# Performance work log

Hardware: AMD Instinct MI355X
Metric: run time of the kernel (lower is better)

## Reference

```python
import jax, jax.numpy as jnp
import numpy as np

B, C, D, Hh, W = 2, 320, 4, 16, 16
N = D * Hh * W          # 1024 nodes
NH = 8                  # num_heads
DH = C // NH            # 40
L = 2                   # num_layers
A, EPD = 16, 64         # da_prior tokens, encode_prior_dim
EDGE_SCALE = 32 ** -0.5 # GraphEdgeFeature dim_head=32
SCALE = DH ** -0.5
EPS = 1e-5


def _ln(x, g, b):
    m = x.mean(-1, keepdims=True)
    v = ((x - m) ** 2).mean(-1, keepdims=True)
    return (x - m) * jax.lax.rsqrt(v + EPS) * g + b


def setup_inputs() -> dict:
    key = jax.random.key(0)
    ks = jax.random.split(key, 16)
    std = 0.02 / np.sqrt(L)
    inp = {
        'x': jax.random.normal(ks[0], (B, C, D, Hh, W), jnp.float32),
        'da_prior': jax.random.normal(ks[1], (B, A, EPD), jnp.float32),
        # GraphEdgeFeature.to_qk (no bias), init std 0.02/sqrt(24)
        'qk_w': jax.random.normal(ks[2], (2 * C, C), jnp.float32) * (0.02 / np.sqrt(24)),
        # fc_prior
        'fcp_w': jax.random.normal(ks[3], (C, EPD), jnp.float32) * 0.02,
        'fcp_b': jnp.zeros((C,), jnp.float32),
        # per-layer (stacked over L)
        'ln1_g': jnp.ones((L, C), jnp.float32),
        'ln1_b': jnp.zeros((L, C), jnp.float32),
        'gln_g': jnp.ones((L, C), jnp.float32),
        'gln_b': jnp.zeros((L, C), jnp.float32),
        'qkv_w': jax.random.normal(ks[4], (L, 3 * C, C), jnp.float32) * std,
        'qkv_b': jnp.zeros((L, 3 * C), jnp.float32),
        'proj_w': jax.random.normal(ks[5], (L, C, C), jnp.float32) * std,
        'proj_b': jnp.zeros((L, C), jnp.float32),
        # expand Conv2d(1, NH, 1): weight [NH], bias [NH]
        'exp_w': jax.random.normal(ks[6], (L, NH), jnp.float32),
        'exp_b': jnp.zeros((L, NH), jnp.float32),
        # reduce Conv2d(NH, 1, 1): weight [NH], bias scalar
        'red_w': jax.random.normal(ks[7], (L, NH), jnp.float32) / np.sqrt(NH),
        'red_b': jnp.zeros((L,), jnp.float32),
    }
    return inp


def _forward(x, da_prior, qk_w, fcp_w, fcp_b, ln1_g, ln1_b, gln_g, gln_b,
             qkv_w, qkv_b, proj_w, proj_b, exp_w, exp_b, red_w, red_b):
    node = x.reshape(B, C, N)                       # [B,C,N]
    # ---- GraphEdgeFeature: full-dim QK attention over nodes ----
    xt = node.transpose(0, 2, 1)                    # [B,N,C]
    qk = xt @ qk_w.T                                # [B,N,2C]
    q_e, k_e = jnp.split(qk, 2, axis=-1)
    edge = jax.nn.softmax(jnp.einsum('bqc,bkc->bqk', q_e, k_e) * EDGE_SCALE, axis=-1)  # [B,N,N]
    # ---- fc_prior ----
    da = da_prior @ fcp_w.T + fcp_b                 # [B,A,C]
    s = da.sum(axis=1)                              # [B,C] (sum over 'a' in einsum bnc,bca->bnc)
    for l in range(L):
        # block norm1 over channel dim
        nt = _ln(node.transpose(0, 2, 1), ln1_g[l], ln1_b[l])   # [B,N,C]
        # torch.einsum('bnn,bnc->bnc') takes the DIAGONAL of edge
        diag = jnp.diagonal(edge, axis1=1, axis2=2)             # [B,N]
        node2 = diag[:, :, None] * nt * s[:, None, :] + nt      # [B,N,C]
        y = _ln(node2, gln_g[l], gln_b[l])
        qkv = (y @ qkv_w[l].T + qkv_b[l]).reshape(B, N, 3, NH, DH)
        qkv = qkv.transpose(2, 0, 3, 1, 4)                      # [3,B,H,N,DH]
        q, k, v = qkv[0], qkv[1], qkv[2]
        attn = jnp.einsum('bhnd,bhmd->bhnm', q, k) * SCALE
        attn = attn + edge[:, None] * exp_w[l][None, :, None, None] + exp_b[l][None, :, None, None]
        a = jax.nn.softmax(attn, axis=-1)                       # [B,H,N,N]
        node_out = jnp.einsum('bhnm,bhmd->bhnd', a, v).transpose(0, 2, 1, 3).reshape(B, N, C)
        edge_new = jnp.einsum('bhnm,h->bnm', a + attn, red_w[l]) + red_b[l]  # [B,N,N]
        ws = jax.nn.softmax(edge_new, axis=-1)
        wsum = (ws * edge_new).sum(-1)                          # [B,N]
        node_out = node_out + wsum[:, :, None]                  # fc=Identity, broadcast
        node_out = node_out @ proj_w[l].T + proj_b[l]
        node = node_out.transpose(0, 2, 1)                      # [B,C,N]
        edge = edge + edge_new
    return node.reshape(B, C, D, Hh, W)


def reference(x, da_prior, qk_w, fcp_w, fcp_b, ln1_g, ln1_b, gln_g, gln_b,
              qkv_w, qkv_b, proj_w, proj_b, exp_w, exp_b, red_w, red_b):
    return _forward(x, da_prior, qk_w, fcp_w, fcp_b, ln1_g, ln1_b, gln_g, gln_b,
                    qkv_w, qkv_b, proj_w, proj_b, exp_w, exp_b, red_w, red_b)
```

## Files before the change

### kernel.cpp

```cpp
#include <hip/hip_runtime.h>
#include <math.h>

#define EDGE_SCALE 0.17677669529663687f
#define ATT_SCALE  0.15811388300841897f
#define LN_EPS 1e-5f

typedef __attribute__((ext_vector_type(8))) short bf8;
typedef __attribute__((ext_vector_type(4))) float f32x4;

__device__ __forceinline__ f32x4 mfma16(bf8 a, bf8 b, f32x4 c) {
  return __builtin_amdgcn_mfma_f32_16x16x32_bf16(a, b, c, 0, 0, 0);
}
__device__ __forceinline__ unsigned short f2bf(float f) {
  union { float f; unsigned u; } v; v.f = f;
  unsigned r = v.u + 0x7FFF + ((v.u >> 16) & 1);
  return (unsigned short)(r >> 16);
}
__device__ __forceinline__ float bf2f(unsigned short h) {
  union { unsigned u; float f; } v; v.u = ((unsigned)h) << 16;
  return v.f;
}
__device__ __forceinline__ float wave_max(float v) {
  #pragma unroll
  for (int o = 32; o > 0; o >>= 1) v = fmaxf(v, __shfl_xor(v, o));
  return v;
}
__device__ __forceinline__ float wave_sum(float v) {
  #pragma unroll
  for (int o = 32; o > 0; o >>= 1) v += __shfl_xor(v, o);
  return v;
}

__global__ __launch_bounds__(256) void k_trans(const float* __restrict__ x,
    float* __restrict__ node, unsigned short* __restrict__ nodebf) {
  __shared__ float tile[32][33];
  const int b = blockIdx.z;
  const int n0 = blockIdx.x * 32, c0 = blockIdx.y * 32;
  const int tx = threadIdx.x & 31, ty = threadIdx.x >> 5;
  #pragma unroll
  for (int k = 0; k < 4; ++k) {
    int c = c0 + ty + 8 * k;
    tile[ty + 8 * k][tx] = x[((size_t)b * 320 + c) * 1024 + n0 + tx];
  }
  __syncthreads();
  #pragma unroll
  for (int k = 0; k < 4; ++k) {
    int n = n0 + ty + 8 * k;
    float v = tile[tx][ty + 8 * k];
    size_t idx = ((size_t)b * 1024 + n) * 320 + c0 + tx;
    node[idx] = v;
    nodebf[idx] = f2bf(v);
  }
}

__global__ __launch_bounds__(320) void k_svec(const float* __restrict__ da,
    const float* __restrict__ fw, const float* __restrict__ fb, float* __restrict__ sv) {
  __shared__ float ds[64];
  const int b = blockIdx.x, t = threadIdx.x;
  if (t < 64) {
    float a = 0.f;
    #pragma unroll
    for (int i = 0; i < 16; ++i) a += da[b * 1024 + i * 64 + t];
    ds[t] = a;
  }
  __syncthreads();
  if (t < 320) {
    float acc = 16.f * fb[t];
    #pragma unroll
    for (int e = 0; e < 64; ++e) acc = fmaf(ds[e], fw[t * 64 + e], acc);
    sv[b * 320 + t] = acc;
  }
}

__global__ void k_wcvt(const float* __restrict__ a, int na,
                       const float* __restrict__ b, int nb,
                       const float* __restrict__ c, int nc,
                       unsigned short* __restrict__ out) {
  int tot = na + nb + nc;
  for (int i = blockIdx.x * blockDim.x + threadIdx.x; i < tot; i += gridDim.x * blockDim.x) {
    float v = (i < na) ? a[i] : ((i < na + nb) ? b[i - na] : c[i - na - nb]);
    out[i] = f2bf(v);
  }
}

__global__ __launch_bounds__(256, 4) void k_mgemm(
    const unsigned short* __restrict__ A, const unsigned short* __restrict__ W,
    const float* __restrict__ bias, void* p0, void* p1, void* p2, int mode) {
  __shared__ float smem[64 * 65];
  const int t = threadIdx.x, w = t >> 6, lane = t & 63;
  const int q16 = lane >> 4, l16 = lane & 15;
  const int rt = blockIdx.x * 64, jt = blockIdx.y * 64;
  f32x4 acc[4];
  #pragma unroll
  for (int i = 0; i < 4; ++i)
    #pragma unroll
    for (int j = 0; j < 4; ++j) acc[i][j] = 0.f;
  const unsigned short* ap = A + (size_t)(rt + 16 * w + l16) * 320 + q16 * 8;
  const unsigned short* wp = W + (size_t)(jt + l16) * 320 + q16 * 8;
  for (int kc = 0; kc < 10; ++kc) {
    bf8 af = *(const bf8*)(ap + kc * 32);
    #pragma unroll
    for (int ct = 0; ct < 4; ++ct) {
      bf8 bf = *(const bf8*)(wp + (size_t)ct * 16 * 320 + kc * 32);
      acc[ct] = mfma16(af, bf, acc[ct]);
    }
  }
  if (mode == 0 || mode == 1) {
    #pragma unroll
    for (int ct = 0; ct < 4; ++ct) {
      int col = jt + ct * 16 + l16;
      float bv = bias ? bias[col] : 0.f;
      #pragma unroll
      for (int r = 0; r < 4; ++r) {
        int row = rt + 16 * w + q16 * 4 + r;
        float v = acc[ct][r] + bv;
        if (mode == 0) {
          ((float*)p0)[(size_t)row * 320 + col] = v;
        } else {
          if (col < 320) ((unsigned short*)p0)[(size_t)row * 320 + col] = f2bf(v);
          else           ((unsigned short*)p1)[(size_t)row * 320 + col - 320] = f2bf(v);
        }
      }
    }
  } else if (mode == 2) {
    const int part = jt / 320;
    if (part < 2) {
      unsigned short* dst = (unsigned short*)(part == 0 ? p0 : p1);
      #pragma unroll
      for (int ct = 0; ct < 4; ++ct) {
        int col = jt + ct * 16 + l16;
        float bv = bias[col];
        int rem = col - part * 320;
        int h = rem / 40, d = rem % 40;
        #pragma unroll
        for (int r = 0; r < 4; ++r) {
          int row = rt + 16 * w + q16 * 4 + r;
          int b = row >> 10, n = row & 1023;
          size_t base = (((size_t)b * 8 + h) * 1024 + n) * 64;
          dst[base + d] = f2bf(acc[ct][r] + bv);
          if (d < 24) dst[base + 40 + d] = 0;
        }
      }
    } else {
      unsigned short* vt_t = (unsigned short*)smem;
      #pragma unroll
      for (int ct = 0; ct < 4; ++ct) {
        int col = jt + ct * 16 + l16;
        float bv = bias[col];
        #pragma unroll
        for (int r = 0; r < 4; ++r)
          vt_t[(ct * 16 + l16) * 72 + 16 * w + q16 * 4 + r] = f2bf(acc[ct][r] + bv);
      }
      __syncthreads();
      const int cl = t >> 2, seg = t & 3;
      int rem = (jt - 640) + cl;
      int h = rem / 40, d = rem % 40;
      int b = rt >> 10, n = (rt & 1023) + seg * 16;
      const float4* lp = (const float4*)&vt_t[cl * 72 + seg * 16];
      float4 a0 = lp[0], a1 = lp[1];
      float4* gp = (float4*)((unsigned short*)p2 +
                             (((size_t)b * 8 + h) * 48 + d) * 1024 + n);
      gp[0] = a0; gp[1] = a1;
    }
  } else {
    #pragma unroll
    for (int ct = 0; ct < 4; ++ct) {
      int col = jt + ct * 16 + l16;
      float bv = bias[col];
      #pragma unroll
      for (int r = 0; r < 4; ++r)
        smem[(16 * w + q16 * 4 + r) * 65 + ct * 16 + l16] = acc[ct][r] + bv;
    }
    __syncthreads();
    const int cl = t >> 2, seg = t & 3;
    int b = rt >> 10, n = (rt & 1023) + seg * 16;
    float* orow = (float*)p0 + ((size_t)b * 320 + jt + cl) * 1024 + n;
    #pragma unroll
    for (int i2 = 0; i2 < 4; ++i2) {
      float4 vv;
      vv.x = smem[(seg * 16 + i2 * 4 + 0) * 65 + cl];
      vv.y = smem[(seg * 16 + i2 * 4 + 1) * 65 + cl];
      vv.z = smem[(seg * 16 + i2 * 4 + 2) * 65 + cl];
      vv.w = smem[(seg * 16 + i2 * 4 + 3) * 65 + cl];
      ((float4*)orow)[i2] = vv;
    }
  }
}

__global__ __launch_bounds__(256, 4) void k_sgemm(
    const unsigned short* __restrict__ qe, const unsigned short* __restrict__ ke,
    float* __restrict__ S) {
  const int t = threadIdx.x, w = t >> 6, lane = t & 63;
  const int q16 = lane >> 4, l16 = lane & 15;
  const int rt = blockIdx.x * 64, jt = blockIdx.y * 64, b = blockIdx.z;
  const unsigned short* A = qe + (size_t)b * 1024 * 320;
  const unsigned short* W = ke + (size_t)b * 1024 * 320;
  f32x4 acc[4];
  #pragma unroll
  for (int i = 0; i < 4; ++i)
    #pragma unroll
    for (int j = 0; j < 4; ++j) acc[i][j] = 0.f;
  const unsigned short* ap = A + (size_t)(rt + 16 * w + l16) * 320 + q16 * 8;
  const unsigned short* wp = W + (size_t)(jt + l16) * 320 + q16 * 8;
  for (int kc = 0; kc < 10; ++kc) {
    bf8 af = *(const bf8*)(ap + kc * 32);
    #pragma unroll
    for (int ct = 0; ct < 4; ++ct) {
      bf8 bf = *(const bf8*)(wp + (size_t)ct * 16 * 320 + kc * 32);
      acc[ct] = mfma16(af, bf, acc[ct]);
    }
  }
  #pragma unroll
  for (int ct = 0; ct < 4; ++ct)
    #pragma unroll
    for (int r = 0; r < 4; ++r)
      S[((size_t)b * 1024 + rt + 16 * w + q16 * 4 + r) * 1024 + jt + ct * 16 + l16] =
          acc[ct][r] * EDGE_SCALE;
}

__global__ __launch_bounds__(256) void k_smax(const float* __restrict__ S,
                                              float* __restrict__ edge) {
  const int w = threadIdx.x >> 6, lane = threadIdx.x & 63;
  const int row = blockIdx.x * 4 + w;
  const float4* sp = (const float4*)(S + (size_t)row * 1024) + lane;
  float4 v[4];
  #pragma unroll
  for (int i = 0; i < 4; ++i) v[i] = sp[i * 64];
  float mx = -3.4e38f;
  #pragma unroll
  for (int i = 0; i < 4; ++i)
    mx = fmaxf(mx, fmaxf(fmaxf(v[i].x, v[i].y), fmaxf(v[i].z, v[i].w)));
  mx = wave_max(mx);
  float s = 0.f;
  #pragma unroll
  for (int i = 0; i < 4; ++i) {
    v[i].x = __expf(v[i].x - mx); v[i].y = __expf(v[i].y - mx);
    v[i].z = __expf(v[i].z - mx); v[i].w = __expf(v[i].w - mx);
    s += v[i].x + v[i].y + v[i].z + v[i].w;
  }
  s = wave_sum(s);
  float inv = 1.f / s;
  float4* ep = (float4*)(edge + (size_t)row * 1024) + lane;
  #pragma unroll
  for (int i = 0; i < 4; ++i)
    ep[i * 64] = make_float4(v[i].x * inv, v[i].y * inv, v[i].z * inv, v[i].w * inv);
}

__global__ __launch_bounds__(256) void k_ln(const float* __restrict__ node,
    const float* __restrict__ edge, const float* __restrict__ sv,
    const float* __restrict__ g1, const float* __restrict__ b1,
    const float* __restrict__ g2, const float* __restrict__ b2,
    unsigned short* __restrict__ y) {
  const int w = threadIdx.x >> 6, lane = threadIdx.x & 63;
  const int row = blockIdx.x * 4 + w;
  const int b = row >> 10, n = row & 1023;
  const float* xr = node + (size_t)row * 320;
  float x[5];
  #pragma unroll
  for (int i = 0; i < 5; ++i) x[i] = xr[lane + 64 * i];
  float s = x[0] + x[1] + x[2] + x[3] + x[4];
  float mean = wave_sum(s) * (1.f / 320.f);
  float v = 0.f;
  #pragma unroll
  for (int i = 0; i < 5; ++i) { float d = x[i] - mean; v += d * d; }
  float rstd = rsqrtf(wave_sum(v) * (1.f / 320.f) + LN_EPS);
  float diag = edge[(size_t)row * 1024 + n];
  float n2[5];
  #pragma unroll
  for (int i = 0; i < 5; ++i) {
    int c = lane + 64 * i;
    float nt = (x[i] - mean) * rstd * g1[c] + b1[c];
    n2[i] = diag * nt * sv[b * 320 + c] + nt;
  }
  s = n2[0] + n2[1] + n2[2] + n2[3] + n2[4];
  float mean2 = wave_sum(s) * (1.f / 320.f);
  v = 0.f;
  #pragma unroll
  for (int i = 0; i < 5; ++i) { float d = n2[i] - mean2; v += d * d; }
  float rstd2 = rsqrtf(wave_sum(v) * (1.f / 320.f) + LN_EPS);
  unsigned short* yr = y + (size_t)row * 320;
  #pragma unroll
  for (int i = 0; i < 5; ++i) {
    int c = lane + 64 * i;
    yr[c] = f2bf((n2[i] - mean2) * rstd2 * g2[c] + b2[c]);
  }
}

__global__ __launch_bounds__(256, 4) void k_score(
    const unsigned short* __restrict__ qbf, const unsigned short* __restrict__ kbf,
    const unsigned short* __restrict__ vtb, const float* __restrict__ edge,
    unsigned short* __restrict__ thbuf, float* __restrict__ att,
    const float* __restrict__ ew, const float* __restrict__ eb,
    const float* __restrict__ rw) {
  __shared__ unsigned short a_lds[4][4][16][20];
  __shared__ unsigned short th_lds[4][16][72];
  __shared__ float ored[4][3][16][17];
  __shared__ float redm[4][16], reds[4][16];
  const int t = threadIdx.x, w = t >> 6, lane = t & 63;
  const int q16 = lane >> 4, l16 = lane & 15;
  const int n0 = blockIdx.x * 16, h = blockIdx.y, b = blockIdx.z;
  const size_t bh = (size_t)b * 8 + h;
  const unsigned short* qp = qbf + (bh * 1024 + n0 + l16) * 64 + q16 * 8;
  bf8 af0 = *(const bf8*)(qp);
  bf8 af1 = *(const bf8*)(qp + 32);
  f32x4 acc[16];
  #pragma unroll
  for (int i = 0; i < 16; ++i)
    #pragma unroll
    for (int j = 0; j < 4; ++j) acc[i][j] = 0.f;
  const unsigned short* kp = kbf + (bh * 1024 + (size_t)w * 256 + l16) * 64 + q16 * 8;
  #pragma unroll
  for (int tt = 0; tt < 16; ++tt) {
    const unsigned short* kpt = kp + (size_t)tt * 16 * 64;
    bf8 b0 = *(const bf8*)(kpt);
    bf8 b1 = *(const bf8*)(kpt + 32);
    acc[tt] = mfma16(af0, b0, acc[tt]);
    acc[tt] = mfma16(af1, b1, acc[tt]);
  }
  const float ewh = ew[h], ebh = eb[h], rwh = rw[h];
  const float* ep = edge + ((size_t)b * 1024 + n0 + q16 * 4) * 1024 + w * 256 + l16;
  #pragma unroll
  for (int tt = 0; tt < 16; ++tt)
    #pragma unroll
    for (int r = 0; r < 4; ++r) {
      float ev = ep[(size_t)r * 1024 + tt * 16];
      acc[tt][r] = fmaf(acc[tt][r], ATT_SCALE, fmaf(ev, ewh, ebh));
    }
  float pm[4] = {-3.4e38f, -3.4e38f, -3.4e38f, -3.4e38f};
  #pragma unroll
  for (int tt = 0; tt < 16; ++tt)
    #pragma unroll
    for (int r = 0; r < 4; ++r) pm[r] = fmaxf(pm[r], acc[tt][r]);
  #pragma unroll
  for (int r = 0; r < 4; ++r)
    #pragma unroll
    for (int o = 1; o <= 8; o <<= 1) pm[r] = fmaxf(pm[r], __shfl_xor(pm[r], o));
  if (l16 == 0) {
    #pragma unroll
    for (int r = 0; r < 4; ++r) redm[w][q16 * 4 + r] = pm[r];
  }
  __syncthreads();
  float m[4], ps[4] = {0.f, 0.f, 0.f, 0.f};
  #pragma unroll
  for (int r = 0; r < 4; ++r)
    m[r] = fmaxf(fmaxf(redm[0][q16 * 4 + r], redm[1][q16 * 4 + r]),
                 fmaxf(redm[2][q16 * 4 + r], redm[3][q16 * 4 + r]));
  #pragma unroll
  for (int tt = 0; tt < 16; ++tt)
    #pragma unroll
    for (int r = 0; r < 4; ++r) ps[r] += __expf(acc[tt][r] - m[r]);
  #pragma unroll
  for (int r = 0; r < 4; ++r)
    #pragma unroll
    for (int o = 1; o <= 8; o <<= 1) ps[r] += __shfl_xor(ps[r], o);
  if (l16 == 0) {
    #pragma unroll
    for (int r = 0; r < 4; ++r) reds[w][q16 * 4 + r] = ps[r];
  }
  __syncthreads();
  float inv[4];
  #pragma unroll
  for (int r = 0; r < 4; ++r)
    inv[r] = 1.f / (reds[0][q16 * 4 + r] + reds[1][q16 * 4 + r] +
                    reds[2][q16 * 4 + r] + reds[3][q16 * 4 + r]);
  f32x4 oacc[3];
  #pragma unroll
  for (int i = 0; i < 3; ++i)
    #pragma unroll
    for (int j = 0; j < 4; ++j) oacc[i][j] = 0.f;
  unsigned short* tbase = thbuf + (bh * 1024 + n0) * 1024 + w * 256;
  const int trow = lane >> 2, tc4 = lane & 3;
  #pragma unroll
  for (int g = 0; g < 4; ++g) {
    #pragma unroll
    for (int ti = 0; ti < 4; ++ti) {
      int tt = g * 4 + ti;
      #pragma unroll
      for (int r = 0; r < 4; ++r) {
        float e = __expf(acc[tt][r] - m[r]);
        float a = e * inv[r];
        a_lds[w][ti][q16 * 4 + r][l16] = f2bf(a);
        th_lds[w][q16 * 4 + r][ti * 16 + l16] = f2bf(rwh * (a + acc[tt][r]));
      }
    }
    #pragma unroll
    for (int kk = 0; kk < 2; ++kk) {
      const unsigned short* ap2 = &a_lds[w][kk * 2 + (q16 >> 1)][l16][(q16 & 1) * 8];
      short4 lo = *(const short4*)(ap2);
      short4 hi = *(const short4*)(ap2 + 4);
      bf8 afv = {lo.x, lo.y, lo.z, lo.w, hi.x, hi.y, hi.z, hi.w};
      int kc = w * 8 + g * 2 + kk;
      const unsigned short* vp = vtb + (bh * 48 + l16) * 1024 + (size_t)kc * 32 + q16 * 8;
      #pragma unroll
      for (int nt = 0; nt < 3; ++nt) {
        bf8 bfv = *(const bf8*)(vp + (size_t)nt * 16 * 1024);
        oacc[nt] = mfma16(afv, bfv, oacc[nt]);
      }
    }
    {
      const float4* lp = (const float4*)&th_lds[w][trow][tc4 * 16];
      float4 v0 = lp[0], v1 = lp[1];
      float4* gp = (float4*)(tbase + (size_t)trow * 1024 + g * 64 + tc4 * 16);
      gp[0] = v0; gp[1] = v1;
    }
  }
  #pragma unroll
  for (int nt = 0; nt < 3; ++nt)
    #pragma unroll
    for (int r = 0; r < 4; ++r) ored[w][nt][q16 * 4 + r][l16] = oacc[nt][r];
  __syncthreads();
  #pragma unroll
  for (int k = 0; k < 3; ++k) {
    int o = k * 256 + t;
    int nt = o >> 8, row = (o >> 4) & 15, col = o & 15;
    int dim = nt * 16 + col;
    float sum = ored[0][nt][row][col] + ored[1][nt][row][col] +
                ored[2][nt][row][col] + ored[3][nt][row][col];
    if (dim < 40)
      att[((size_t)b * 1024 + n0 + row) * 320 + h * 40 + dim] = sum;
  }
}

__global__ __launch_bounds__(256) void k_wsum(
    const unsigned short* __restrict__ thbuf, float* __restrict__ edge,
    const float* __restrict__ att, unsigned short* __restrict__ attbf,
    const float* __restrict__ rb) {
  const int w = threadIdx.x >> 6, lane = threadIdx.x & 63;
  const int row = blockIdx.x * 4 + w;
  const int b = row >> 10, n = row & 1023;
  const float rbv = rb[0];
  float tv[16];
  #pragma unroll
  for (int i = 0; i < 16; ++i) tv[i] = rbv;
  #pragma unroll 1
  for (int h = 0; h < 8; ++h) {
    const unsigned short* tph = thbuf + (((size_t)b * 8 + h) * 1024 + n) * 1024 + lane * 4;
    #pragma unroll
    for (int seg = 0; seg < 4; ++seg) {
      ushort4 u = *(const ushort4*)(tph + seg * 256);
      tv[seg * 4 + 0] += bf2f(u.x);
      tv[seg * 4 + 1] += bf2f(u.y);
      tv[seg * 4 + 2] += bf2f(u.z);
      tv[seg * 4 + 3] += bf2f(u.w);
    }
  }
  float4* erp = (float4*)(edge + ((size_t)b * 1024 + n) * 1024) + lane;
  #pragma unroll
  for (int seg = 0; seg < 4; ++seg) {
    float4 e = erp[seg * 64];
    e.x += tv[seg * 4 + 0]; e.y += tv[seg * 4 + 1];
    e.z += tv[seg * 4 + 2]; e.w += tv[seg * 4 + 3];
    erp[seg * 64] = e;
  }
  float mx = -3.4e38f;
  #pragma unroll
  for (int i = 0; i < 16; ++i) mx = fmaxf(mx, tv[i]);
  mx = wave_max(mx);
  float s = 0.f, num = 0.f;
  #pragma unroll
  for (int i = 0; i < 16; ++i) {
    float e = __expf(tv[i] - mx);
    s += e; num += e * tv[i];
  }
  s = wave_sum(s); num = wave_sum(num);
  const float wsum = num / s;
  const float* ar = att + (size_t)row * 320;
  unsigned short* ao = attbf + (size_t)row * 320;
  #pragma unroll
  for (int i = 0; i < 5; ++i) {
    int c = lane + 64 * i;
    ao[c] = f2bf(ar[c] + wsum);
  }
}

extern "C" void kernel_launch(void* const* d_in, const int* in_sizes, int n_in,
                              void* d_out, int out_size, void* d_ws, size_t ws_size,
                              hipStream_t stream) {
  const float* x      = (const float*)d_in[0];
  const float* da     = (const float*)d_in[1];
  const float* qk_w   = (const float*)d_in[2];
  const float* fcp_w  = (const float*)d_in[3];
  const float* fcp_b  = (const float*)d_in[4];
  const float* ln1_g  = (const float*)d_in[5];
  const float* ln1_b  = (const float*)d_in[6];
  const float* gln_g  = (const float*)d_in[7];
  const float* gln_b  = (const float*)d_in[8];
  const float* qkv_w  = (const float*)d_in[9];
  const float* qkv_b  = (const float*)d_in[10];
  const float* proj_w = (const float*)d_in[11];
  const float* proj_b = (const float*)d_in[12];
  const float* exp_w  = (const float*)d_in[13];
  const float* exp_b  = (const float*)d_in[14];
  const float* red_w  = (const float*)d_in[15];
  const float* red_b  = (const float*)d_in[16];
  float* ws = (float*)d_ws;
  float* node  = ws + 0;
  unsigned short* ybf   = (unsigned short*)(ws + 655360);
  float* attb  = ws + 983040;
  unsigned short* attbf = (unsigned short*)(ws + 1638400);
  float* edge  = ws + 1966080;
  float* svec  = ws + 4063232;
  unsigned short* nodebf = (unsigned short*)(ws + 4063872);
  unsigned short* qe   = (unsigned short*)(ws + 4391552);
  unsigned short* ke   = (unsigned short*)(ws + 4719232);
  unsigned short* qbf  = (unsigned short*)(ws + 5046912);
  unsigned short* kbf  = (unsigned short*)(ws + 5571200);
  unsigned short* vtb  = (unsigned short*)(ws + 6095488);
  unsigned short* wbf  = (unsigned short*)(ws + 6488704);
  unsigned short* thbuf= (unsigned short*)(ws + 7000704);
  float* sbuf = ws + 15389312;
  float* out = (float*)d_out;
  unsigned short* qk_wb   = wbf;
  unsigned short* qkv_wb  = wbf + 204800;
  unsigned short* proj_wb = wbf + 819200;

  hipLaunchKernelGGL(k_trans, dim3(32, 10, 2), dim3(256), 0, stream, x, node, nodebf);
  hipLaunchKernelGGL(k_svec, dim3(2), dim3(320), 0, stream, da, fcp_w, fcp_b, svec);
  hipLaunchKernelGGL(k_wcvt, dim3(512), dim3(256), 0, stream,
                     qk_w, 204800, qkv_w, 614400, proj_w, 204800, wbf);
  hipLaunchKernelGGL(k_mgemm, dim3(32, 10), dim3(256), 0, stream,
                     nodebf, qk_wb, (const float*)nullptr, qe, ke, (void*)nullptr, 1);
  hipLaunchKernelGGL(k_sgemm, dim3(16, 16, 2), dim3(256), 0, stream, qe, ke, sbuf);
  hipLaunchKernelGGL(k_smax, dim3(512), dim3(256), 0, stream, sbuf, edge);
  for (int l = 0; l < 2; ++l) {
    hipLaunchKernelGGL(k_ln, dim3(512), dim3(256), 0, stream, node, edge, svec,
                       ln1_g + l * 320, ln1_b + l * 320, gln_g + l * 320, gln_b + l * 320, ybf);
    hipLaunchKernelGGL(k_mgemm, dim3(32, 15), dim3(256), 0, stream,
                       ybf, qkv_wb + (size_t)l * 307200, qkv_b + l * 960, qbf, kbf, vtb, 2);
    hipLaunchKernelGGL(k_score, dim3(64, 8, 2), dim3(256), 0, stream,
                       qbf, kbf, vtb, edge, thbuf, attb,
                       exp_w + l * 8, exp_b + l * 8, red_w + l * 8);
    hipLaunchKernelGGL(k_wsum, dim3(512), dim3(256), 0, stream,
                       thbuf, edge, attb, attbf, red_b + l);
    if (l == 0)
      hipLaunchKernelGGL(k_mgemm, dim3(32, 5), dim3(256), 0, stream,
                         attbf, proj_wb, proj_b, node, (void*)nullptr, (void*)nullptr, 0);
    else
      hipLaunchKernelGGL(k_mgemm, dim3(32, 5), dim3(256), 0, stream,
                         attbf, proj_wb + 102400, proj_b + 320, out,
                         (void*)nullptr, (void*)nullptr, 3);
  }
}
```

Measured before the change: 293.5 us.

## Fuse edge score GEMM with softmax, pair heads in score kernel, drop max pass

The initial edge QK GEMM and its row softmax are fused into one kernel, so the fp32 score matrix is never written to or read back from memory. The score kernel now handles two heads per block and sums their reduce-weighted contributions in registers, which halves the per-head intermediate traffic into the weighted-sum kernel. Both softmaxes skip the max-subtraction pass, removing one reduction and barrier, at the risk of exp overflow if scores are large. Zeroing of the q/k head padding moves from every GEMM epilogue into a one-time clear inside the weight-conversion kernel.

```diff
diff --git a/kernel.cpp b/kernel.cpp
--- a/kernel.cpp
+++ b/kernel.cpp
@@ -75,12 +75,16 @@
 __global__ void k_wcvt(const float* __restrict__ a, int na,
                        const float* __restrict__ b, int nb,
                        const float* __restrict__ c, int nc,
-                       unsigned short* __restrict__ out) {
+                       unsigned short* __restrict__ out,
+                       uint4* __restrict__ zbuf, int zn4) {
   int tot = na + nb + nc;
   for (int i = blockIdx.x * blockDim.x + threadIdx.x; i < tot; i += gridDim.x * blockDim.x) {
     float v = (i < na) ? a[i] : ((i < na + nb) ? b[i - na] : c[i - na - nb]);
     out[i] = f2bf(v);
   }
+  const uint4 z = {0u, 0u, 0u, 0u};
+  for (int i = blockIdx.x * blockDim.x + threadIdx.x; i < zn4; i += gridDim.x * blockDim.x)
+    zbuf[i] = z;
 }
 
 __global__ __launch_bounds__(256, 4) void k_mgemm(
@@ -136,9 +140,7 @@
         for (int r = 0; r < 4; ++r) {
           int row = rt + 16 * w + q16 * 4 + r;
           int b = row >> 10, n = row & 1023;
-          size_t base = (((size_t)b * 8 + h) * 1024 + n) * 64;
-          dst[base + d] = f2bf(acc[ct][r] + bv);
-          if (d < 24) dst[base + 40 + d] = 0;
+          dst[(((size_t)b * 8 + h) * 1024 + n) * 64 + d] = f2bf(acc[ct][r] + bv);
         }
       }
     } else {
@@ -187,63 +189,64 @@
   }
 }
 
-__global__ __launch_bounds__(256, 4) void k_sgemm(
+__global__ __launch_bounds__(512, 2) void k_edge3(
     const unsigned short* __restrict__ qe, const unsigned short* __restrict__ ke,
-    float* __restrict__ S) {
+    float* __restrict__ edge) {
+  __shared__ float zred[8][16];
   const int t = threadIdx.x, w = t >> 6, lane = t & 63;
   const int q16 = lane >> 4, l16 = lane & 15;
-  const int rt = blockIdx.x * 64, jt = blockIdx.y * 64, b = blockIdx.z;
-  const unsigned short* A = qe + (size_t)b * 1024 * 320;
-  const unsigned short* W = ke + (size_t)b * 1024 * 320;
-  f32x4 acc[4];
-  #pragma unroll
-  for (int i = 0; i < 4; ++i)
+  const int n0 = blockIdx.x * 16, b = blockIdx.y;
+  const unsigned short* qp = qe + ((size_t)(b * 1024 + n0 + l16)) * 320 + q16 * 8;
+  bf8 af[10];
+  #pragma unroll
+  for (int kc = 0; kc < 10; ++kc) af[kc] = *(const bf8*)(qp + kc * 32);
+  f32x4 acc[8];
+  #pragma unroll
+  for (int i = 0; i < 8; ++i)
     #pragma unroll
     for (int j = 0; j < 4; ++j) acc[i][j] = 0.f;
-  const unsigned short* ap = A + (size_t)(rt + 16 * w + l16) * 320 + q16 * 8;
-  const unsigned short* wp = W + (size_t)(jt + l16) * 320 + q16 * 8;
-  for (int kc = 0; kc < 10; ++kc) {
-    bf8 af = *(const bf8*)(ap + kc * 32);
-    #pragma unroll
-    for (int ct = 0; ct < 4; ++ct) {
-      bf8 bf = *(const bf8*)(wp + (size_t)ct * 16 * 320 + kc * 32);
-      acc[ct] = mfma16(af, bf, acc[ct]);
-    }
-  }
-  #pragma unroll
-  for (int ct = 0; ct < 4; ++ct)
-    #pragma unroll
-    for (int r = 0; r < 4; ++r)
-      S[((size_t)b * 1024 + rt + 16 * w + q16 * 4 + r) * 1024 + jt + ct * 16 + l16] =
-          acc[ct][r] * EDGE_SCALE;
-}
-
-__global__ __launch_bounds__(256) void k_smax(const float* __restrict__ S,
-                                              float* __restrict__ edge) {
-  const int w = threadIdx.x >> 6, lane = threadIdx.x & 63;
-  const int row = blockIdx.x * 4 + w;
-  const float4* sp = (const float4*)(S + (size_t)row * 1024) + lane;
-  float4 v[4];
-  #pragma unroll
-  for (int i = 0; i < 4; ++i) v[i] = sp[i * 64];
-  float mx = -3.4e38f;
-  #pragma unroll
-  for (int i = 0; i < 4; ++i)
-    mx = fmaxf(mx, fmaxf(fmaxf(v[i].x, v[i].y), fmaxf(v[i].z, v[i].w)));
-  mx = wave_max(mx);
-  float s = 0.f;
-  #pragma unroll
-  for (int i = 0; i < 4; ++i) {
-    v[i].x = __expf(v[i].x - mx); v[i].y = __expf(v[i].y - mx);
-    v[i].z = __expf(v[i].z - mx); v[i].w = __expf(v[i].w - mx);
-    s += v[i].x + v[i].y + v[i].z + v[i].w;
-  }
-  s = wave_sum(s);
-  float inv = 1.f / s;
-  float4* ep = (float4*)(edge + (size_t)row * 1024) + lane;
-  #pragma unroll
-  for (int i = 0; i < 4; ++i)
-    ep[i * 64] = make_float4(v[i].x * inv, v[i].y * inv, v[i].z * inv, v[i].w * inv);
+  const unsigned short* kp = ke + ((size_t)(b * 1024 + w * 128 + l16)) * 320 + q16 * 8;
+  #pragma unroll
+  for (int mt = 0; mt < 8; ++mt) {
+    const unsigned short* kpt = kp + (size_t)mt * 16 * 320;
+    #pragma unroll
+    for (int kc = 0; kc < 10; ++kc) {
+      bf8 bf = *(const bf8*)(kpt + kc * 32);
+      acc[mt] = mfma16(af[kc], bf, acc[mt]);
+    }
+  }
+  float zp[4] = {0.f, 0.f, 0.f, 0.f};
+  #pragma unroll
+  for (int mt = 0; mt < 8; ++mt)
+    #pragma unroll
+    for (int r = 0; r < 4; ++r) {
+      float e = __expf(acc[mt][r] * EDGE_SCALE);
+      acc[mt][r] = e;
+      zp[r] += e;
+    }
+  #pragma unroll
+  for (int r = 0; r < 4; ++r)
+    #pragma unroll
+    for (int o = 1; o <= 8; o <<= 1) zp[r] += __shfl_xor(zp[r], o);
+  if (l16 == 0) {
+    #pragma unroll
+    for (int r = 0; r < 4; ++r) zred[w][q16 * 4 + r] = zp[r];
+  }
+  __syncthreads();
+  float inv[4];
+  #pragma unroll
+  for (int r = 0; r < 4; ++r) {
+    float s = 0.f;
+    #pragma unroll
+    for (int ww = 0; ww < 8; ++ww) s += zred[ww][q16 * 4 + r];
+    inv[r] = 1.f / s;
+  }
+  #pragma unroll
+  for (int r = 0; r < 4; ++r) {
+    float* ep = edge + ((size_t)(b * 1024 + n0 + q16 * 4 + r)) * 1024 + w * 128 + l16;
+    #pragma unroll
+    for (int mt = 0; mt < 8; ++mt) ep[mt * 16] = acc[mt][r] * inv[r];
+  }
 }
 
 __global__ __launch_bounds__(256) void k_ln(const float* __restrict__ node,
@@ -286,143 +289,139 @@
   }
 }
 
-__global__ __launch_bounds__(256, 4) void k_score(
+__global__ __launch_bounds__(256, 2) void k_score2(
     const unsigned short* __restrict__ qbf, const unsigned short* __restrict__ kbf,
     const unsigned short* __restrict__ vtb, const float* __restrict__ edge,
-    unsigned short* __restrict__ thbuf, float* __restrict__ att,
+    unsigned short* __restrict__ th, float* __restrict__ att,
     const float* __restrict__ ew, const float* __restrict__ eb,
     const float* __restrict__ rw) {
   __shared__ unsigned short a_lds[4][4][16][20];
-  __shared__ unsigned short th_lds[4][16][72];
-  __shared__ float ored[4][3][16][17];
-  __shared__ float redm[4][16], reds[4][16];
+  __shared__ float ored[2][4][3][16][17];
+  __shared__ float zred[2][4][16];
   const int t = threadIdx.x, w = t >> 6, lane = t & 63;
   const int q16 = lane >> 4, l16 = lane & 15;
-  const int n0 = blockIdx.x * 16, h = blockIdx.y, b = blockIdx.z;
-  const size_t bh = (size_t)b * 8 + h;
-  const unsigned short* qp = qbf + (bh * 1024 + n0 + l16) * 64 + q16 * 8;
-  bf8 af0 = *(const bf8*)(qp);
-  bf8 af1 = *(const bf8*)(qp + 32);
-  f32x4 acc[16];
-  #pragma unroll
-  for (int i = 0; i < 16; ++i)
-    #pragma unroll
-    for (int j = 0; j < 4; ++j) acc[i][j] = 0.f;
-  const unsigned short* kp = kbf + (bh * 1024 + (size_t)w * 256 + l16) * 64 + q16 * 8;
-  #pragma unroll
-  for (int tt = 0; tt < 16; ++tt) {
-    const unsigned short* kpt = kp + (size_t)tt * 16 * 64;
-    bf8 b0 = *(const bf8*)(kpt);
-    bf8 b1 = *(const bf8*)(kpt + 32);
-    acc[tt] = mfma16(af0, b0, acc[tt]);
-    acc[tt] = mfma16(af1, b1, acc[tt]);
-  }
-  const float ewh = ew[h], ebh = eb[h], rwh = rw[h];
-  const float* ep = edge + ((size_t)b * 1024 + n0 + q16 * 4) * 1024 + w * 256 + l16;
+  const int n0 = blockIdx.x * 16, hp = blockIdx.y, b = blockIdx.z;
+  float t_reg[16][4];
   #pragma unroll
   for (int tt = 0; tt < 16; ++tt)
     #pragma unroll
-    for (int r = 0; r < 4; ++r) {
-      float ev = ep[(size_t)r * 1024 + tt * 16];
-      acc[tt][r] = fmaf(acc[tt][r], ATT_SCALE, fmaf(ev, ewh, ebh));
-    }
-  float pm[4] = {-3.4e38f, -3.4e38f, -3.4e38f, -3.4e38f};
-  #pragma unroll
-  for (int tt = 0; tt < 16; ++tt)
-    #pragma unroll
-    for (int r = 0; r < 4; ++r) pm[r] = fmaxf(pm[r], acc[tt][r]);
-  #pragma unroll
-  for (int r = 0; r < 4; ++r)
-    #pragma unroll
-    for (int o = 1; o <= 8; o <<= 1) pm[r] = fmaxf(pm[r], __shfl_xor(pm[r], o));
-  if (l16 == 0) {
-    #pragma unroll
-    for (int r = 0; r < 4; ++r) redm[w][q16 * 4 + r] = pm[r];
-  }
+    for (int r = 0; r < 4; ++r) t_reg[tt][r] = 0.f;
+  f32x4 oacc[2][3];
+  #pragma unroll
+  for (int hh = 0; hh < 2; ++hh)
+    #pragma unroll
+    for (int i = 0; i < 3; ++i)
+      #pragma unroll
+      for (int j = 0; j < 4; ++j) oacc[hh][i][j] = 0.f;
+  const float* ep = edge + ((size_t)(b * 1024 + n0 + q16 * 4)) * 1024 + w * 256 + l16;
+  #pragma unroll 1
+  for (int hh = 0; hh < 2; ++hh) {
+    const int h = hp * 2 + hh;
+    const size_t bh = (size_t)b * 8 + h;
+    const float ewh = ew[h], ebh = eb[h], rwh = rw[h];
+    const unsigned short* qp = qbf + (bh * 1024 + n0 + l16) * 64 + q16 * 8;
+    bf8 af0 = *(const bf8*)(qp);
+    bf8 af1 = *(const bf8*)(qp + 32);
+    f32x4 acc[16];
+    #pragma unroll
+    for (int i = 0; i < 16; ++i)
+      #pragma unroll
+      for (int j = 0; j < 4; ++j) acc[i][j] = 0.f;
+    const unsigned short* kp = kbf + (bh * 1024 + (size_t)w * 256 + l16) * 64 + q16 * 8;
+    #pragma unroll
+    for (int tt = 0; tt < 16; ++tt) {
+      const unsigned short* kpt = kp + (size_t)tt * 16 * 64;
+      bf8 b0 = *(const bf8*)(kpt);
+      bf8 b1 = *(const bf8*)(kpt + 32);
+      acc[tt] = mfma16(af0, b0, acc[tt]);
+      acc[tt] = mfma16(af1, b1, acc[tt]);
+    }
+    float zp[4] = {0.f, 0.f, 0.f, 0.f};
+    #pragma unroll
+    for (int tt = 0; tt < 16; ++tt)
+      #pragma unroll
+      for (int r = 0; r < 4; ++r) {
+        float ev = ep[(size_t)r * 1024 + tt * 16];
+        float s = fmaf(acc[tt][r], ATT_SCALE, fmaf(ev, ewh, ebh));
+        acc[tt][r] = s;
+        zp[r] += __expf(s);
+      }
+    #pragma unroll
+    for (int r = 0; r < 4; ++r)
+      #pragma unroll
+      for (int o = 1; o <= 8; o <<= 1) zp[r] += __shfl_xor(zp[r], o);
+    if (l16 == 0) {
+      #pragma unroll
+      for (int r = 0; r < 4; ++r) zred[hh][w][q16 * 4 + r] = zp[r];
+    }
+    __syncthreads();
+    float invZ[4];
+    #pragma unroll
+    for (int r = 0; r < 4; ++r)
+      invZ[r] = 1.f / (zred[hh][0][q16 * 4 + r] + zred[hh][1][q16 * 4 + r] +
+                       zred[hh][2][q16 * 4 + r] + zred[hh][3][q16 * 4 + r]);
+    #pragma unroll
+    for (int g = 0; g < 4; ++g) {
+      #pragma unroll
+      for (int ti = 0; ti < 4; ++ti) {
+        int tt = g * 4 + ti;
+        #pragma unroll
+        for (int r = 0; r < 4; ++r) {
+          float s = acc[tt][r];
+          float e = __expf(s);
+          a_lds[w][ti][q16 * 4 + r][l16] = f2bf(e * invZ[r]);
+          t_reg[tt][r] = fmaf(rwh, fmaf(e, invZ[r], s), t_reg[tt][r]);
+        }
+      }
+      #pragma unroll
+      for (int kk = 0; kk < 2; ++kk) {
+        const unsigned short* ap2 = &a_lds[w][kk * 2 + (q16 >> 1)][l16][(q16 & 1) * 8];
+        short4 lo = *(const short4*)(ap2);
+        short4 hi = *(const short4*)(ap2 + 4);
+        bf8 afv = {lo.x, lo.y, lo.z, lo.w, hi.x, hi.y, hi.z, hi.w};
+        int kc = w * 8 + g * 2 + kk;
+        const unsigned short* vp = vtb + (bh * 48 + l16) * 1024 + (size_t)kc * 32 + q16 * 8;
+        #pragma unroll
+        for (int nt = 0; nt < 3; ++nt) {
+          bf8 bfv = *(const bf8*)(vp + (size_t)nt * 16 * 1024);
+          oacc[hh][nt] = mfma16(afv, bfv, oacc[hh][nt]);
+        }
+      }
+    }
+  }
+  {
+    unsigned short* tp = th + (((size_t)(b * 4 + hp)) * 1024 + n0 + q16 * 4) * 1024
+                         + w * 256 + l16;
+    #pragma unroll
+    for (int tt = 0; tt < 16; ++tt)
+      #pragma unroll
+      for (int r = 0; r < 4; ++r)
+        tp[(size_t)r * 1024 + tt * 16] = f2bf(t_reg[tt][r]);
+  }
+  #pragma unroll
+  for (int hh = 0; hh < 2; ++hh)
+    #pragma unroll
+    for (int nt = 0; nt < 3; ++nt)
+      #pragma unroll
+      for (int r = 0; r < 4; ++r) ored[hh][w][nt][q16 * 4 + r][l16] = oacc[hh][nt][r];
   __syncthreads();
-  float m[4], ps[4] = {0.f, 0.f, 0.f, 0.f};
-  #pragma unroll
-  for (int r = 0; r < 4; ++r)
-    m[r] = fmaxf(fmaxf(redm[0][q16 * 4 + r], redm[1][q16 * 4 + r]),
-                 fmaxf(redm[2][q16 * 4 + r], redm[3][q16 * 4 + r]));
-  #pragma unroll
-  for (int tt = 0; tt < 16; ++tt)
-    #pragma unroll
-    for (int r = 0; r < 4; ++r) ps[r] += __expf(acc[tt][r] - m[r]);
-  #pragma unroll
-  for (int r = 0; r < 4; ++r)
-    #pragma unroll
-    for (int o = 1; o <= 8; o <<= 1) ps[r] += __shfl_xor(ps[r], o);
-  if (l16 == 0) {
-    #pragma unroll
-    for (int r = 0; r < 4; ++r) reds[w][q16 * 4 + r] = ps[r];
-  }
-  __syncthreads();
-  float inv[4];
-  #pragma unroll
-  for (int r = 0; r < 4; ++r)
-    inv[r] = 1.f / (reds[0][q16 * 4 + r] + reds[1][q16 * 4 + r] +
-                    reds[2][q16 * 4 + r] + reds[3][q16 * 4 + r]);
-  f32x4 oacc[3];
-  #pragma unroll
-  for (int i = 0; i < 3; ++i)
-    #pragma unroll
-    for (int j = 0; j < 4; ++j) oacc[i][j] = 0.f;
-  unsigned short* tbase = thbuf + (bh * 1024 + n0) * 1024 + w * 256;
-  const int trow = lane >> 2, tc4 = lane & 3;
-  #pragma unroll
-  for (int g = 0; g < 4; ++g) {
-    #pragma unroll
-    for (int ti = 0; ti < 4; ++ti) {
-      int tt = g * 4 + ti;
-      #pragma unroll
-      for (int r = 0; r < 4; ++r) {
-        float e = __expf(acc[tt][r] - m[r]);
-        float a = e * inv[r];
-        a_lds[w][ti][q16 * 4 + r][l16] = f2bf(a);
-        th_lds[w][q16 * 4 + r][ti * 16 + l16] = f2bf(rwh * (a + acc[tt][r]));
-      }
-    }
-    #pragma unroll
-    for (int kk = 0; kk < 2; ++kk) {
-      const unsigned short* ap2 = &a_lds[w][kk * 2 + (q16 >> 1)][l16][(q16 & 1) * 8];
-      short4 lo = *(const short4*)(ap2);
-      short4 hi = *(const short4*)(ap2 + 4);
-      bf8 afv = {lo.x, lo.y, lo.z, lo.w, hi.x, hi.y, hi.z, hi.w};
-      int kc = w * 8 + g * 2 + kk;
-      const unsigned short* vp = vtb + (bh * 48 + l16) * 1024 + (size_t)kc * 32 + q16 * 8;
-      #pragma unroll
-      for (int nt = 0; nt < 3; ++nt) {
-        bf8 bfv = *(const bf8*)(vp + (size_t)nt * 16 * 1024);
-        oacc[nt] = mfma16(afv, bfv, oacc[nt]);
-      }
-    }
-    {
-      const float4* lp = (const float4*)&th_lds[w][trow][tc4 * 16];
-      float4 v0 = lp[0], v1 = lp[1];
-      float4* gp = (float4*)(tbase + (size_t)trow * 1024 + g * 64 + tc4 * 16);
-      gp[0] = v0; gp[1] = v1;
-    }
-  }
-  #pragma unroll
-  for (int nt = 0; nt < 3; ++nt)
-    #pragma unroll
-    for (int r = 0; r < 4; ++r) ored[w][nt][q16 * 4 + r][l16] = oacc[nt][r];
-  __syncthreads();
-  #pragma unroll
-  for (int k = 0; k < 3; ++k) {
-    int o = k * 256 + t;
-    int nt = o >> 8, row = (o >> 4) & 15, col = o & 15;
-    int dim = nt * 16 + col;
-    float sum = ored[0][nt][row][col] + ored[1][nt][row][col] +
-                ored[2][nt][row][col] + ored[3][nt][row][col];
-    if (dim < 40)
-      att[((size_t)b * 1024 + n0 + row) * 320 + h * 40 + dim] = sum;
+  #pragma unroll
+  for (int hh = 0; hh < 2; ++hh) {
+    #pragma unroll
+    for (int k = 0; k < 3; ++k) {
+      int o = k * 256 + t;
+      int nt = o >> 8, row = (o >> 4) & 15, col = o & 15;
+      int dim = nt * 16 + col;
+      float sum = ored[hh][0][nt][row][col] + ored[hh][1][nt][row][col] +
+                  ored[hh][2][nt][row][col] + ored[hh][3][nt][row][col];
+      if (dim < 40)
+        att[((size_t)b * 1024 + n0 + row) * 320 + (hp * 2 + hh) * 40 + dim] = sum;
+    }
   }
 }
 
 __global__ __launch_bounds__(256) void k_wsum(
-    const unsigned short* __restrict__ thbuf, float* __restrict__ edge,
+    const unsigned short* __restrict__ th, float* __restrict__ edge,
     const float* __restrict__ att, unsigned short* __restrict__ attbf,
     const float* __restrict__ rb) {
   const int w = threadIdx.x >> 6, lane = threadIdx.x & 63;
@@ -433,8 +432,8 @@
   #pragma unroll
   for (int i = 0; i < 16; ++i) tv[i] = rbv;
   #pragma unroll 1
-  for (int h = 0; h < 8; ++h) {
-    const unsigned short* tph = thbuf + (((size_t)b * 8 + h) * 1024 + n) * 1024 + lane * 4;
+  for (int hp = 0; hp < 4; ++hp) {
+    const unsigned short* tph = th + (((size_t)b * 4 + hp) * 1024 + n) * 1024 + lane * 4;
     #pragma unroll
     for (int seg = 0; seg < 4; ++seg) {
       ushort4 u = *(const ushort4*)(tph + seg * 256);
@@ -507,8 +506,7 @@
   unsigned short* kbf  = (unsigned short*)(ws + 5571200);
   unsigned short* vtb  = (unsigned short*)(ws + 6095488);
   unsigned short* wbf  = (unsigned short*)(ws + 6488704);
-  unsigned short* thbuf= (unsigned short*)(ws + 7000704);
-  float* sbuf = ws + 15389312;
+  unsigned short* th   = (unsigned short*)(ws + 7000704);
   float* out = (float*)d_out;
   unsigned short* qk_wb   = wbf;
   unsigned short* qkv_wb  = wbf + 204800;
@@ -517,21 +515,21 @@
   hipLaunchKernelGGL(k_trans, dim3(32, 10, 2), dim3(256), 0, stream, x, node, nodebf);
   hipLaunchKernelGGL(k_svec, dim3(2), dim3(320), 0, stream, da, fcp_w, fcp_b, svec);
   hipLaunchKernelGGL(k_wcvt, dim3(512), dim3(256), 0, stream,
-                     qk_w, 204800, qkv_w, 614400, proj_w, 204800, wbf);
+                     qk_w, 204800, qkv_w, 614400, proj_w, 204800, wbf,
+                     (uint4*)qbf, 262144);
   hipLaunchKernelGGL(k_mgemm, dim3(32, 10), dim3(256), 0, stream,
                      nodebf, qk_wb, (const float*)nullptr, qe, ke, (void*)nullptr, 1);
-  hipLaunchKernelGGL(k_sgemm, dim3(16, 16, 2), dim3(256), 0, stream, qe, ke, sbuf);
-  hipLaunchKernelGGL(k_smax, dim3(512), dim3(256), 0, stream, sbuf, edge);
+  hipLaunchKernelGGL(k_edge3, dim3(64, 2), dim3(512), 0, stream, qe, ke, edge);
   for (int l = 0; l < 2; ++l) {
     hipLaunchKernelGGL(k_ln, dim3(512), dim3(256), 0, stream, node, edge, svec,
                        ln1_g + l * 320, ln1_b + l * 320, gln_g + l * 320, gln_b + l * 320, ybf);
     hipLaunchKernelGGL(k_mgemm, dim3(32, 15), dim3(256), 0, stream,
                        ybf, qkv_wb + (size_t)l * 307200, qkv_b + l * 960, qbf, kbf, vtb, 2);
-    hipLaunchKernelGGL(k_score, dim3(64, 8, 2), dim3(256), 0, stream,
-                       qbf, kbf, vtb, edge, thbuf, attb,
+    hipLaunchKernelGGL(k_score2, dim3(64, 4, 2), dim3(256), 0, stream,
+                       qbf, kbf, vtb, edge, th, attb,
                        exp_w + l * 8, exp_b + l * 8, red_w + l * 8);
     hipLaunchKernelGGL(k_wsum, dim3(512), dim3(256), 0, stream,
-                       thbuf, edge, attb, attbf, red_b + l);
+                       th, edge, attb, attbf, red_b + l);
     if (l == 0)
       hipLaunchKernelGGL(k_mgemm, dim3(32, 5), dim3(256), 0, stream,
                          attbf, proj_wb, proj_b, node, (void*)nullptr, (void*)nullptr, 0);
```

Measured after the change: 340.8 us. +16.1%, slower.
